# Performance work log

Measured on AMD Instinct MI355X. Metric: run time of the kernel, lower is better.

## Reference

```python
import jax, jax.numpy as jnp
import numpy as np

TEMP = 0.5
WEIGHT = (0.4, 0.3, 0.3)


def _l2norm(x):
    n = jnp.linalg.norm(x, axis=-1, keepdims=True)
    return x / jnp.maximum(n, 1e-12)


def _forward(st_i, st_j, car_i, car_j, pl_i, pl_j, gt_labels,
             cen_st, cen_car, cen_pl, conc):
    w = jnp.asarray(WEIGHT, dtype=st_i.dtype)[:, None, None]  # [3,1,1]
    feats = [jnp.concatenate([_l2norm(a), _l2norm(b)], axis=0)
             for a, b in ((st_i, st_j), (car_i, car_j), (pl_i, pl_j))]  # each [N,D]
    sims = jnp.stack([f @ f.T for f in feats])  # [3,N,N]
    wmask = jnp.where(sims == 0, jnp.zeros_like(w), w)
    wsim = (sims * wmask).sum(0) / (wmask.sum(0) + 1e-12)  # [N,N]
    e = jnp.exp(wsim / TEMP)
    N = e.shape[0]
    B = N // 2
    idx = jnp.arange(N)
    pos = e[idx, (idx + B) % N]  # positive_mask gather: one positive per row
    # negative_mask excludes diagonal and the positive -> row sum minus both
    neg_sum = e.sum(-1) - e[idx, idx] - pos
    loss = (-jnp.log(pos / (pos + neg_sum))).mean()

    # prototype branch: gt_labels covers all C clusters, unique set == arange(C)
    labels = gt_labels[:, 0]  # [N]
    C = cen_st.shape[0]
    k = jnp.arange(C - 1)
    neg_ids = k[None, :] + (k[None, :] >= labels[:, None]).astype(k.dtype)  # sorted ids != label
    proto_ids = jnp.concatenate([labels[:, None], neg_ids], axis=1)  # [N,C], col 0 = positive
    logits = jnp.stack([
        jnp.take_along_axis(f @ c.T, proto_ids, axis=1)
        for f, c in zip(feats, (cen_st, cen_car, cen_pl))])  # [3,N,C]
    temp_proto = conc[:, proto_ids]  # [3,N,C]
    logits = logits / (temp_proto + 1e-12)
    w2 = jnp.where((temp_proto == 0) | (logits == 0), jnp.zeros_like(w), w)
    logits_w = (logits * w2).sum(0) / (w2.sum(0) + 1e-12)  # [N,C]
    # CrossEntropyLoss(mean) with target class 0 for every row
    loss_proto = (-jax.nn.log_softmax(logits_w, axis=-1)[:, 0]).mean()
    return loss + loss_proto


def setup_inputs() -> dict:
    key = jax.random.key(0)
    ks = jax.random.split(key, 12)
    B, D, C = 2048, 128, 512
    N = 2 * B
    inp = {}
    names = ['st_feat_i', 'st_feat_j', 'car_feat_i', 'car_feat_j',
             'plate_feat_i', 'plate_feat_j']
    for i, nm in enumerate(names):
        inp[nm] = jax.random.normal(ks[i], (B, D), dtype=jnp.float32)
    # labels covering all C clusters so torch.unique(gt_labels) == arange(C)
    labels = jnp.tile(jnp.arange(C, dtype=jnp.int32), N // C)
    labels = jax.random.permutation(ks[6], labels)
    inp['gt_labels'] = labels[:, None]
    inp['st_centroids'] = jax.random.normal(ks[7], (C, D), dtype=jnp.float32)
    inp['car_centroids'] = jax.random.normal(ks[8], (C, D), dtype=jnp.float32)
    inp['plate_centroids'] = jax.random.normal(ks[9], (C, D), dtype=jnp.float32)
    inp['concentration'] = jax.random.uniform(ks[10], (3, C), dtype=jnp.float32,
                                              minval=0.1, maxval=1.0)
    return inp


def reference(st_feat_i, st_feat_j, car_feat_i, car_feat_j,
              plate_feat_i, plate_feat_j, gt_labels,
              st_centroids, car_centroids, plate_centroids, concentration):
    return _forward(st_feat_i, st_feat_j, car_feat_i, car_feat_j,
                    plate_feat_i, plate_feat_j, gt_labels,
                    st_centroids, car_centroids, plate_centroids, concentration)
```

## Files before the change

### kernel.cpp

```cpp
#include <hip/hip_runtime.h>
#include <hip/hip_bf16.h>
#include <math.h>

#define BB 2048
#define NN 4096
#define DD 128
#define CC 512

typedef __attribute__((ext_vector_type(8))) short bf16x8;
typedef __attribute__((ext_vector_type(4))) float f32x4;

__global__ __launch_bounds__(256) void k_normprep(
    const float* __restrict__ si, const float* __restrict__ sj,
    const float* __restrict__ ci, const float* __restrict__ cj,
    const float* __restrict__ pi, const float* __restrict__ pj,
    const float* __restrict__ cst, const float* __restrict__ cca,
    const float* __restrict__ cpl, const float* __restrict__ conc,
    __hip_bfloat16* __restrict__ fbf, __hip_bfloat16* __restrict__ cbf) {
  const int m   = blockIdx.y;
  const int tid = threadIdx.x;
  const int w   = tid >> 6;
  const int t   = tid & 63;
  const float sqw = (m == 0) ? 0.632455532033676f : 0.547722557505166f;
  if (blockIdx.x < NN / 4) {
    const int row = blockIdx.x * 4 + w;
    const float* src;
    if (m == 0)      src = (row < BB) ? si : sj;
    else if (m == 1) src = (row < BB) ? ci : cj;
    else             src = (row < BB) ? pi : pj;
    const int r = (row < BB) ? row : row - BB;
    float2 v = ((const float2*)(src + (size_t)r * DD))[t];
    float ss = v.x * v.x + v.y * v.y;
    #pragma unroll
    for (int k = 32; k >= 1; k >>= 1) ss += __shfl_xor(ss, k);
    const float inv = sqw / fmaxf(sqrtf(ss), 1e-12f);
    __hip_bfloat16* db = fbf + (size_t)m * NN * DD + (size_t)row * DD;
    db[2 * t]     = __float2bfloat16(v.x * inv);
    db[2 * t + 1] = __float2bfloat16(v.y * inv);
  } else {
    const int crow = (blockIdx.x - NN / 4) * 4 + w;
    const float* src = (m == 0) ? cst : (m == 1) ? cca : cpl;
    const float sc = sqw / (conc[m * CC + crow] + 1e-12f);
    float2 v = ((const float2*)(src + (size_t)crow * DD))[t];
    __hip_bfloat16* db = cbf + (size_t)m * CC * DD + (size_t)crow * DD;
    db[2 * t]     = __float2bfloat16(v.x * sc);
    db[2 * t + 1] = __float2bfloat16(v.y * sc);
  }
}

__global__ __launch_bounds__(256, 3) void k_sim(const __hip_bfloat16* __restrict__ fbf,
                                                float* __restrict__ rowsum,
                                                float* __restrict__ pos_e,
                                                float* __restrict__ diag_e) {
  __shared__ bf16x8 As[1024];
  __shared__ bf16x8 Bs[1024];

  int tB = blockIdx.x;
  int by = 0;
  while (tB >= 32 - by) { tB -= 32 - by; ++by; }
  const int bx = by + tB;
  const bool diag = (by == bx);
  const int rowBase = by * 128;
  const int colBase = bx * 128;

  const int tid  = threadIdx.x;
  const int lane = tid & 63;
  const int wid  = tid >> 6;
  const int wr   = wid >> 1, wc = wid & 1;
  const int l15  = lane & 15;
  const int kg   = lane >> 4;

  const int srow = tid >> 3;
  const int kc   = tid & 7;
  const int sc   = kc ^ (srow & 7);

  f32x4 acc[4][4] = {};
  bf16x8 ra[4], rb[4];

  {
    const __hip_bfloat16* F = fbf;
    #pragma unroll
    for (int q = 0; q < 4; ++q) {
      ra[q] = *(const bf16x8*)(F + (size_t)(rowBase + q * 32 + srow) * DD + kc * 8);
      if (!diag)
        rb[q] = *(const bf16x8*)(F + (size_t)(colBase + q * 32 + srow) * DD + kc * 8);
    }
  }

  for (int t = 0; t < 6; ++t) {
    #pragma unroll
    for (int q = 0; q < 4; ++q) {
      As[(q * 32 + srow) * 8 + sc] = ra[q];
      if (!diag) Bs[(q * 32 + srow) * 8 + sc] = rb[q];
    }
    __syncthreads();

    if (t < 5) {
      const __hip_bfloat16* F = fbf + (size_t)((t + 1) >> 1) * NN * DD + ((t + 1) & 1) * 64;
      #pragma unroll
      for (int q = 0; q < 4; ++q) {
        ra[q] = *(const bf16x8*)(F + (size_t)(rowBase + q * 32 + srow) * DD + kc * 8);
        if (!diag)
          rb[q] = *(const bf16x8*)(F + (size_t)(colBase + q * 32 + srow) * DD + kc * 8);
      }
    }

    const bf16x8* Bsrc = diag ? As : Bs;
    #pragma unroll
    for (int ks2 = 0; ks2 < 2; ++ks2) {
      bf16x8 a[4], b[4];
      const int ch = (ks2 * 4 + kg) ^ (l15 & 7);
      #pragma unroll
      for (int ti = 0; ti < 4; ++ti)
        a[ti] = As[(wr * 64 + ti * 16 + l15) * 8 + ch];
      #pragma unroll
      for (int tj = 0; tj < 4; ++tj)
        b[tj] = Bsrc[(wc * 64 + tj * 16 + l15) * 8 + ch];
      #pragma unroll
      for (int ti = 0; ti < 4; ++ti)
        #pragma unroll
        for (int tj = 0; tj < 4; ++tj)
          acc[ti][tj] = __builtin_amdgcn_mfma_f32_16x16x32_bf16(a[ti], b[tj], acc[ti][tj], 0, 0, 0);
    }
    __syncthreads();
  }

  float csum[4] = {0.f, 0.f, 0.f, 0.f};
  #pragma unroll
  for (int ti = 0; ti < 4; ++ti) {
    #pragma unroll
    for (int j = 0; j < 4; ++j) {
      const int i = rowBase + wr * 64 + ti * 16 + kg * 4 + j;
      float rsum = 0.f;
      #pragma unroll
      for (int tj = 0; tj < 4; ++tj) {
        const int jcol = colBase + wc * 64 + tj * 16 + l15;
        const float e = expf(2.0f * acc[ti][tj][j]);
        rsum += e;
        csum[tj] += e;
        if (diag) {
          if (jcol == i) diag_e[i] = e;
        } else if (jcol == ((i + BB) & (NN - 1))) {
          pos_e[i] = e;
          pos_e[jcol] = e;
        }
      }
      #pragma unroll
      for (int msk = 8; msk >= 1; msk >>= 1) rsum += __shfl_xor(rsum, msk);
      if (l15 == 0) atomicAdd(&rowsum[i], rsum);
    }
  }
  if (!diag) {
    #pragma unroll
    for (int tj = 0; tj < 4; ++tj) {
      float v = csum[tj];
      v += __shfl_xor(v, 16);
      v += __shfl_xor(v, 32);
      if (lane < 16) atomicAdd(&rowsum[colBase + wc * 64 + tj * 16 + l15], v);
    }
  }
}

__global__ __launch_bounds__(256) void k_proto2(const __hip_bfloat16* __restrict__ fbf,
                                                const __hip_bfloat16* __restrict__ cbf,
                                                const int* __restrict__ labels,
                                                float* __restrict__ lossB) {
  __shared__ int   slab[16];
  __shared__ float wmax[4][16], wsum[4][16], zlab[16];
  const int tid  = threadIdx.x;
  const int lane = tid & 63;
  const int w    = tid >> 6;
  const int l15  = lane & 15;
  const int kg   = lane >> 4;
  const int row0 = blockIdx.x * 16;

  if (tid < 16) slab[tid] = labels[row0 + tid];
  __syncthreads();

  f32x4 acc[8] = {};
  #pragma unroll
  for (int ks = 0; ks < 12; ++ks) {
    const int koff = (ks & 3) * 32 + kg * 8;
    const __hip_bfloat16* F  = fbf + (size_t)(ks >> 2) * NN * DD + koff;
    const __hip_bfloat16* Cm = cbf + (size_t)(ks >> 2) * CC * DD + koff;
    const bf16x8 af = *(const bf16x8*)(F + (size_t)(row0 + l15) * DD);
    bf16x8 bf_[8];
    #pragma unroll
    for (int tj = 0; tj < 8; ++tj)
      bf_[tj] = *(const bf16x8*)(Cm + (size_t)(w * 128 + tj * 16 + l15) * DD);
    #pragma unroll
    for (int tj = 0; tj < 8; ++tj)
      acc[tj] = __builtin_amdgcn_mfma_f32_16x16x32_bf16(af, bf_[tj], acc[tj], 0, 0, 0);
  }

  #pragma unroll
  for (int j = 0; j < 4; ++j) {
    const int r = kg * 4 + j;
    #pragma unroll
    for (int tj = 0; tj < 8; ++tj) {
      const int c = w * 128 + tj * 16 + l15;
      if (c == slab[r]) zlab[r] = acc[tj][j];
    }
  }

  #pragma unroll
  for (int j = 0; j < 4; ++j) {
    float mx = acc[0][j];
    #pragma unroll
    for (int tj = 1; tj < 8; ++tj) mx = fmaxf(mx, acc[tj][j]);
    #pragma unroll
    for (int msk = 8; msk >= 1; msk >>= 1) mx = fmaxf(mx, __shfl_xor(mx, msk));
    if (l15 == 0) wmax[w][kg * 4 + j] = mx;
  }
  __syncthreads();

  #pragma unroll
  for (int j = 0; j < 4; ++j) {
    const int r = kg * 4 + j;
    const float bmx = fmaxf(fmaxf(wmax[0][r], wmax[1][r]), fmaxf(wmax[2][r], wmax[3][r]));
    float se = 0.f;
    #pragma unroll
    for (int tj = 0; tj < 8; ++tj) se += expf(acc[tj][j] - bmx);
    #pragma unroll
    for (int msk = 8; msk >= 1; msk >>= 1) se += __shfl_xor(se, msk);
    if (l15 == 0) wsum[w][r] = se;
  }
  __syncthreads();

  if (tid < 16) {
    const int r = tid;
    const float bmx = fmaxf(fmaxf(wmax[0][r], wmax[1][r]), fmaxf(wmax[2][r], wmax[3][r]));
    const float s = wsum[0][r] + wsum[1][r] + wsum[2][r] + wsum[3][r];
    lossB[row0 + r] = bmx + logf(s) - zlab[r];
  }
}

__global__ void k_final(const float* __restrict__ rowsum, const float* __restrict__ pos_e,
                        const float* __restrict__ diag_e, const float* __restrict__ lossB,
                        float* __restrict__ out) {
  __shared__ float redA[4], redB[4];
  const int tid = threadIdx.x;
  float sa = 0.f, sb = 0.f;
  for (int i = tid; i < NN; i += 256) {
    sa += logf(rowsum[i] - diag_e[i]) - logf(pos_e[i]);
    sb += lossB[i];
  }
  const int lane = tid & 63, wv = tid >> 6;
  #pragma unroll
  for (int k = 32; k >= 1; k >>= 1) { sa += __shfl_xor(sa, k); sb += __shfl_xor(sb, k); }
  if (lane == 0) { redA[wv] = sa; redB[wv] = sb; }
  __syncthreads();
  if (tid == 0) {
    const float la = redA[0] + redA[1] + redA[2] + redA[3];
    const float lb = redB[0] + redB[1] + redB[2] + redB[3];
    out[0] = la / (float)NN + lb / (float)NN;
  }
}

extern "C" void kernel_launch(void* const* d_in, const int* in_sizes, int n_in,
                              void* d_out, int out_size, void* d_ws, size_t ws_size,
                              hipStream_t stream) {
  (void)in_sizes; (void)n_in; (void)out_size; (void)ws_size;
  const float* si  = (const float*)d_in[0];
  const float* sj  = (const float*)d_in[1];
  const float* ci  = (const float*)d_in[2];
  const float* cj  = (const float*)d_in[3];
  const float* pi  = (const float*)d_in[4];
  const float* pj  = (const float*)d_in[5];
  const int*   lab = (const int*)d_in[6];
  const float* cst = (const float*)d_in[7];
  const float* cca = (const float*)d_in[8];
  const float* cpl = (const float*)d_in[9];
  const float* cnc = (const float*)d_in[10];

  float* ws     = (float*)d_ws;
  float* rowsum = ws;
  float* pos_e  = rowsum + NN;
  float* diag_e = pos_e + NN;
  float* lossB  = diag_e + NN;
  __hip_bfloat16* fbf = (__hip_bfloat16*)(lossB + NN);
  __hip_bfloat16* cbf = fbf + (size_t)3 * NN * DD;

  hipMemsetAsync(rowsum, 0, NN * sizeof(float), stream);

  k_normprep<<<dim3(NN / 4 + CC / 4, 3), 256, 0, stream>>>(si, sj, ci, cj, pi, pj,
                                                           cst, cca, cpl, cnc, fbf, cbf);
  k_sim<<<528, 256, 0, stream>>>(fbf, rowsum, pos_e, diag_e);
  k_proto2<<<NN / 16, 256, 0, stream>>>(fbf, cbf, lab, lossB);
  k_final<<<1, 256, 0, stream>>>(rowsum, pos_e, diag_e, lossB, (float*)d_out);
}
```

Measured before the change: 127.9 us.

## Merge similarity and prototype kernels into one launch with split-column partial softmax

The separate similarity-GEMM and prototype kernels are fused into one launch. Block IDs below 528 do the similarity tiles and the rest do prototype logits, so the prototype work can fill CUs left idle by the 528 similarity blocks. Each prototype block now covers half of the 512 centroid columns, which doubles the block count. It writes a partial max and sum-of-exp, and the final kernel merges the two halves with a log-sum-exp combine. This removes one kernel launch and boundary at the cost of extra workspace and a little more final-reduction work.

```diff
diff --git a/kernel.cpp b/kernel.cpp
--- a/kernel.cpp
+++ b/kernel.cpp
@@ -6,6 +6,7 @@
 #define NN 4096
 #define DD 128
 #define CC 512
+#define NSIM 528
 
 typedef __attribute__((ext_vector_type(8))) short bf16x8;
 typedef __attribute__((ext_vector_type(4))) float f32x4;
@@ -48,55 +49,43 @@
   }
 }
 
-__global__ __launch_bounds__(256, 3) void k_sim(const __hip_bfloat16* __restrict__ fbf,
-                                                float* __restrict__ rowsum,
-                                                float* __restrict__ pos_e,
-                                                float* __restrict__ diag_e) {
+__global__ __launch_bounds__(256, 3) void k_main(const __hip_bfloat16* __restrict__ fbf,
+                                                 const __hip_bfloat16* __restrict__ cbf,
+                                                 const int* __restrict__ labels,
+                                                 float* __restrict__ rowsum,
+                                                 float* __restrict__ pos_e,
+                                                 float* __restrict__ diag_e,
+                                                 float* __restrict__ pmax_g,
+                                                 float* __restrict__ psum_g,
+                                                 float* __restrict__ zl_g) {
   __shared__ bf16x8 As[1024];
   __shared__ bf16x8 Bs[1024];
-
-  int tB = blockIdx.x;
-  int by = 0;
-  while (tB >= 32 - by) { tB -= 32 - by; ++by; }
-  const int bx = by + tB;
-  const bool diag = (by == bx);
-  const int rowBase = by * 128;
-  const int colBase = bx * 128;
 
   const int tid  = threadIdx.x;
   const int lane = tid & 63;
   const int wid  = tid >> 6;
-  const int wr   = wid >> 1, wc = wid & 1;
   const int l15  = lane & 15;
   const int kg   = lane >> 4;
 
-  const int srow = tid >> 3;
-  const int kc   = tid & 7;
-  const int sc   = kc ^ (srow & 7);
-
-  f32x4 acc[4][4] = {};
-  bf16x8 ra[4], rb[4];
-
-  {
-    const __hip_bfloat16* F = fbf;
-    #pragma unroll
-    for (int q = 0; q < 4; ++q) {
-      ra[q] = *(const bf16x8*)(F + (size_t)(rowBase + q * 32 + srow) * DD + kc * 8);
-      if (!diag)
-        rb[q] = *(const bf16x8*)(F + (size_t)(colBase + q * 32 + srow) * DD + kc * 8);
-    }
-  }
-
-  for (int t = 0; t < 6; ++t) {
-    #pragma unroll
-    for (int q = 0; q < 4; ++q) {
-      As[(q * 32 + srow) * 8 + sc] = ra[q];
-      if (!diag) Bs[(q * 32 + srow) * 8 + sc] = rb[q];
-    }
-    __syncthreads();
-
-    if (t < 5) {
-      const __hip_bfloat16* F = fbf + (size_t)((t + 1) >> 1) * NN * DD + ((t + 1) & 1) * 64;
+  if (blockIdx.x < NSIM) {
+    int tB = blockIdx.x;
+    int by = 0;
+    while (tB >= 32 - by) { tB -= 32 - by; ++by; }
+    const int bx = by + tB;
+    const bool diag = (by == bx);
+    const int rowBase = by * 128;
+    const int colBase = bx * 128;
+
+    const int wr = wid >> 1, wc = wid & 1;
+    const int srow = tid >> 3;
+    const int kc   = tid & 7;
+    const int sc   = kc ^ (srow & 7);
+
+    f32x4 acc[4][4] = {};
+    bf16x8 ra[4], rb[4];
+
+    {
+      const __hip_bfloat16* F = fbf;
       #pragma unroll
       for (int q = 0; q < 4; ++q) {
         ra[q] = *(const bf16x8*)(F + (size_t)(rowBase + q * 32 + srow) * DD + kc * 8);
@@ -105,145 +94,167 @@
       }
     }
 
-    const bf16x8* Bsrc = diag ? As : Bs;
-    #pragma unroll
-    for (int ks2 = 0; ks2 < 2; ++ks2) {
-      bf16x8 a[4], b[4];
-      const int ch = (ks2 * 4 + kg) ^ (l15 & 7);
-      #pragma unroll
-      for (int ti = 0; ti < 4; ++ti)
-        a[ti] = As[(wr * 64 + ti * 16 + l15) * 8 + ch];
+    for (int t = 0; t < 6; ++t) {
+      #pragma unroll
+      for (int q = 0; q < 4; ++q) {
+        As[(q * 32 + srow) * 8 + sc] = ra[q];
+        if (!diag) Bs[(q * 32 + srow) * 8 + sc] = rb[q];
+      }
+      __syncthreads();
+
+      if (t < 5) {
+        const __hip_bfloat16* F = fbf + (size_t)((t + 1) >> 1) * NN * DD + ((t + 1) & 1) * 64;
+        #pragma unroll
+        for (int q = 0; q < 4; ++q) {
+          ra[q] = *(const bf16x8*)(F + (size_t)(rowBase + q * 32 + srow) * DD + kc * 8);
+          if (!diag)
+            rb[q] = *(const bf16x8*)(F + (size_t)(colBase + q * 32 + srow) * DD + kc * 8);
+        }
+      }
+
+      const bf16x8* Bsrc = diag ? As : Bs;
+      #pragma unroll
+      for (int ks2 = 0; ks2 < 2; ++ks2) {
+        bf16x8 a[4], b[4];
+        const int ch = (ks2 * 4 + kg) ^ (l15 & 7);
+        #pragma unroll
+        for (int ti = 0; ti < 4; ++ti)
+          a[ti] = As[(wr * 64 + ti * 16 + l15) * 8 + ch];
+        #pragma unroll
+        for (int tj = 0; tj < 4; ++tj)
+          b[tj] = Bsrc[(wc * 64 + tj * 16 + l15) * 8 + ch];
+        #pragma unroll
+        for (int ti = 0; ti < 4; ++ti)
+          #pragma unroll
+          for (int tj = 0; tj < 4; ++tj)
+            acc[ti][tj] = __builtin_amdgcn_mfma_f32_16x16x32_bf16(a[ti], b[tj], acc[ti][tj], 0, 0, 0);
+      }
+      __syncthreads();
+    }
+
+    float csum[4] = {0.f, 0.f, 0.f, 0.f};
+    #pragma unroll
+    for (int ti = 0; ti < 4; ++ti) {
+      #pragma unroll
+      for (int j = 0; j < 4; ++j) {
+        const int i = rowBase + wr * 64 + ti * 16 + kg * 4 + j;
+        float rsum = 0.f;
+        #pragma unroll
+        for (int tj = 0; tj < 4; ++tj) {
+          const int jcol = colBase + wc * 64 + tj * 16 + l15;
+          const float e = expf(2.0f * acc[ti][tj][j]);
+          rsum += e;
+          csum[tj] += e;
+          if (diag) {
+            if (jcol == i) diag_e[i] = e;
+          } else if (jcol == ((i + BB) & (NN - 1))) {
+            pos_e[i] = e;
+            pos_e[jcol] = e;
+          }
+        }
+        #pragma unroll
+        for (int msk = 8; msk >= 1; msk >>= 1) rsum += __shfl_xor(rsum, msk);
+        if (l15 == 0) atomicAdd(&rowsum[i], rsum);
+      }
+    }
+    if (!diag) {
+      #pragma unroll
+      for (int tj = 0; tj < 4; ++tj) {
+        float v = csum[tj];
+        v += __shfl_xor(v, 16);
+        v += __shfl_xor(v, 32);
+        if (lane < 16) atomicAdd(&rowsum[colBase + wc * 64 + tj * 16 + l15], v);
+      }
+    }
+  } else {
+    float* wmaxs = (float*)As;
+    float* wsums = wmaxs + 64;
+    int*   slab  = (int*)(wsums + 64);
+
+    const int bidp = blockIdx.x - NSIM;
+    const int half = bidp & 1;
+    const int row0 = (bidp >> 1) * 16;
+    const int cbase = half * 256 + wid * 64;
+
+    if (tid < 16) slab[tid] = labels[row0 + tid];
+    __syncthreads();
+
+    f32x4 acc[4] = {};
+    #pragma unroll
+    for (int ks = 0; ks < 12; ++ks) {
+      const int koff = (ks & 3) * 32 + kg * 8;
+      const __hip_bfloat16* F  = fbf + (size_t)(ks >> 2) * NN * DD + koff;
+      const __hip_bfloat16* Cm = cbf + (size_t)(ks >> 2) * CC * DD + koff;
+      const bf16x8 af = *(const bf16x8*)(F + (size_t)(row0 + l15) * DD);
+      bf16x8 bf_[4];
       #pragma unroll
       for (int tj = 0; tj < 4; ++tj)
-        b[tj] = Bsrc[(wc * 64 + tj * 16 + l15) * 8 + ch];
-      #pragma unroll
-      for (int ti = 0; ti < 4; ++ti)
-        #pragma unroll
-        for (int tj = 0; tj < 4; ++tj)
-          acc[ti][tj] = __builtin_amdgcn_mfma_f32_16x16x32_bf16(a[ti], b[tj], acc[ti][tj], 0, 0, 0);
+        bf_[tj] = *(const bf16x8*)(Cm + (size_t)(cbase + tj * 16 + l15) * DD);
+      #pragma unroll
+      for (int tj = 0; tj < 4; ++tj)
+        acc[tj] = __builtin_amdgcn_mfma_f32_16x16x32_bf16(af, bf_[tj], acc[tj], 0, 0, 0);
+    }
+
+    #pragma unroll
+    for (int j = 0; j < 4; ++j) {
+      const int r = kg * 4 + j;
+      #pragma unroll
+      for (int tj = 0; tj < 4; ++tj) {
+        const int c = cbase + tj * 16 + l15;
+        if (c == slab[r]) zl_g[row0 + r] = acc[tj][j];
+      }
+    }
+
+    #pragma unroll
+    for (int j = 0; j < 4; ++j) {
+      float mx = acc[0][j];
+      #pragma unroll
+      for (int tj = 1; tj < 4; ++tj) mx = fmaxf(mx, acc[tj][j]);
+      #pragma unroll
+      for (int msk = 8; msk >= 1; msk >>= 1) mx = fmaxf(mx, __shfl_xor(mx, msk));
+      if (l15 == 0) wmaxs[wid * 16 + kg * 4 + j] = mx;
     }
     __syncthreads();
-  }
-
-  float csum[4] = {0.f, 0.f, 0.f, 0.f};
-  #pragma unroll
-  for (int ti = 0; ti < 4; ++ti) {
+
     #pragma unroll
     for (int j = 0; j < 4; ++j) {
-      const int i = rowBase + wr * 64 + ti * 16 + kg * 4 + j;
-      float rsum = 0.f;
-      #pragma unroll
-      for (int tj = 0; tj < 4; ++tj) {
-        const int jcol = colBase + wc * 64 + tj * 16 + l15;
-        const float e = expf(2.0f * acc[ti][tj][j]);
-        rsum += e;
-        csum[tj] += e;
-        if (diag) {
-          if (jcol == i) diag_e[i] = e;
-        } else if (jcol == ((i + BB) & (NN - 1))) {
-          pos_e[i] = e;
-          pos_e[jcol] = e;
-        }
-      }
-      #pragma unroll
-      for (int msk = 8; msk >= 1; msk >>= 1) rsum += __shfl_xor(rsum, msk);
-      if (l15 == 0) atomicAdd(&rowsum[i], rsum);
-    }
-  }
-  if (!diag) {
-    #pragma unroll
-    for (int tj = 0; tj < 4; ++tj) {
-      float v = csum[tj];
-      v += __shfl_xor(v, 16);
-      v += __shfl_xor(v, 32);
-      if (lane < 16) atomicAdd(&rowsum[colBase + wc * 64 + tj * 16 + l15], v);
+      const int r = kg * 4 + j;
+      const float bmx = fmaxf(fmaxf(wmaxs[0 * 16 + r], wmaxs[1 * 16 + r]),
+                              fmaxf(wmaxs[2 * 16 + r], wmaxs[3 * 16 + r]));
+      float se = 0.f;
+      #pragma unroll
+      for (int tj = 0; tj < 4; ++tj) se += expf(acc[tj][j] - bmx);
+      #pragma unroll
+      for (int msk = 8; msk >= 1; msk >>= 1) se += __shfl_xor(se, msk);
+      if (l15 == 0) wsums[wid * 16 + r] = se;
+    }
+    __syncthreads();
+
+    if (tid < 16) {
+      const int r = tid;
+      const float bmx = fmaxf(fmaxf(wmaxs[0 * 16 + r], wmaxs[1 * 16 + r]),
+                              fmaxf(wmaxs[2 * 16 + r], wmaxs[3 * 16 + r]));
+      const float s = wsums[0 * 16 + r] + wsums[1 * 16 + r] +
+                      wsums[2 * 16 + r] + wsums[3 * 16 + r];
+      pmax_g[(size_t)half * NN + row0 + r] = bmx;
+      psum_g[(size_t)half * NN + row0 + r] = s;
     }
   }
 }
 
-__global__ __launch_bounds__(256) void k_proto2(const __hip_bfloat16* __restrict__ fbf,
-                                                const __hip_bfloat16* __restrict__ cbf,
-                                                const int* __restrict__ labels,
-                                                float* __restrict__ lossB) {
-  __shared__ int   slab[16];
-  __shared__ float wmax[4][16], wsum[4][16], zlab[16];
-  const int tid  = threadIdx.x;
-  const int lane = tid & 63;
-  const int w    = tid >> 6;
-  const int l15  = lane & 15;
-  const int kg   = lane >> 4;
-  const int row0 = blockIdx.x * 16;
-
-  if (tid < 16) slab[tid] = labels[row0 + tid];
-  __syncthreads();
-
-  f32x4 acc[8] = {};
-  #pragma unroll
-  for (int ks = 0; ks < 12; ++ks) {
-    const int koff = (ks & 3) * 32 + kg * 8;
-    const __hip_bfloat16* F  = fbf + (size_t)(ks >> 2) * NN * DD + koff;
-    const __hip_bfloat16* Cm = cbf + (size_t)(ks >> 2) * CC * DD + koff;
-    const bf16x8 af = *(const bf16x8*)(F + (size_t)(row0 + l15) * DD);
-    bf16x8 bf_[8];
-    #pragma unroll
-    for (int tj = 0; tj < 8; ++tj)
-      bf_[tj] = *(const bf16x8*)(Cm + (size_t)(w * 128 + tj * 16 + l15) * DD);
-    #pragma unroll
-    for (int tj = 0; tj < 8; ++tj)
-      acc[tj] = __builtin_amdgcn_mfma_f32_16x16x32_bf16(af, bf_[tj], acc[tj], 0, 0, 0);
-  }
-
-  #pragma unroll
-  for (int j = 0; j < 4; ++j) {
-    const int r = kg * 4 + j;
-    #pragma unroll
-    for (int tj = 0; tj < 8; ++tj) {
-      const int c = w * 128 + tj * 16 + l15;
-      if (c == slab[r]) zlab[r] = acc[tj][j];
-    }
-  }
-
-  #pragma unroll
-  for (int j = 0; j < 4; ++j) {
-    float mx = acc[0][j];
-    #pragma unroll
-    for (int tj = 1; tj < 8; ++tj) mx = fmaxf(mx, acc[tj][j]);
-    #pragma unroll
-    for (int msk = 8; msk >= 1; msk >>= 1) mx = fmaxf(mx, __shfl_xor(mx, msk));
-    if (l15 == 0) wmax[w][kg * 4 + j] = mx;
-  }
-  __syncthreads();
-
-  #pragma unroll
-  for (int j = 0; j < 4; ++j) {
-    const int r = kg * 4 + j;
-    const float bmx = fmaxf(fmaxf(wmax[0][r], wmax[1][r]), fmaxf(wmax[2][r], wmax[3][r]));
-    float se = 0.f;
-    #pragma unroll
-    for (int tj = 0; tj < 8; ++tj) se += expf(acc[tj][j] - bmx);
-    #pragma unroll
-    for (int msk = 8; msk >= 1; msk >>= 1) se += __shfl_xor(se, msk);
-    if (l15 == 0) wsum[w][r] = se;
-  }
-  __syncthreads();
-
-  if (tid < 16) {
-    const int r = tid;
-    const float bmx = fmaxf(fmaxf(wmax[0][r], wmax[1][r]), fmaxf(wmax[2][r], wmax[3][r]));
-    const float s = wsum[0][r] + wsum[1][r] + wsum[2][r] + wsum[3][r];
-    lossB[row0 + r] = bmx + logf(s) - zlab[r];
-  }
-}
-
 __global__ void k_final(const float* __restrict__ rowsum, const float* __restrict__ pos_e,
-                        const float* __restrict__ diag_e, const float* __restrict__ lossB,
+                        const float* __restrict__ diag_e, const float* __restrict__ pmax_g,
+                        const float* __restrict__ psum_g, const float* __restrict__ zl_g,
                         float* __restrict__ out) {
   __shared__ float redA[4], redB[4];
   const int tid = threadIdx.x;
   float sa = 0.f, sb = 0.f;
   for (int i = tid; i < NN; i += 256) {
     sa += logf(rowsum[i] - diag_e[i]) - logf(pos_e[i]);
-    sb += lossB[i];
+    const float m0 = pmax_g[i], m1 = pmax_g[NN + i];
+    const float M = fmaxf(m0, m1);
+    const float s = psum_g[i] * expf(m0 - M) + psum_g[NN + i] * expf(m1 - M);
+    sb += M + logf(s) - zl_g[i];
   }
   const int lane = tid & 63, wv = tid >> 6;
   #pragma unroll
@@ -277,15 +288,17 @@
   float* rowsum = ws;
   float* pos_e  = rowsum + NN;
   float* diag_e = pos_e + NN;
-  float* lossB  = diag_e + NN;
-  __hip_bfloat16* fbf = (__hip_bfloat16*)(lossB + NN);
+  float* pmax_g = diag_e + NN;
+  float* psum_g = pmax_g + 2 * NN;
+  float* zl_g   = psum_g + 2 * NN;
+  __hip_bfloat16* fbf = (__hip_bfloat16*)(zl_g + NN);
   __hip_bfloat16* cbf = fbf + (size_t)3 * NN * DD;
 
   hipMemsetAsync(rowsum, 0, NN * sizeof(float), stream);
 
   k_normprep<<<dim3(NN / 4 + CC / 4, 3), 256, 0, stream>>>(si, sj, ci, cj, pi, pj,
                                                            cst, cca, cpl, cnc, fbf, cbf);
-  k_sim<<<528, 256, 0, stream>>>(fbf, rowsum, pos_e, diag_e);
-  k_proto2<<<NN / 16, 256, 0, stream>>>(fbf, cbf, lab, lossB);
-  k_final<<<1, 256, 0, stream>>>(rowsum, pos_e, diag_e, lossB, (float*)d_out);
+  k_main<<<NSIM + 2 * (NN / 16), 256, 0, stream>>>(fbf, cbf, lab, rowsum, pos_e, diag_e,
+                                                   pmax_g, psum_g, zl_g);
+  k_final<<<1, 256, 0, stream>>>(rowsum, pos_e, diag_e, pmax_g, psum_g, zl_g, (float*)d_out);
 }
```

Result: no change. 126.9 us (-0.8%).
